# Kernel tuning notes

Measured on AMD Instinct MI355X. Metric: run time of the kernel, lower is better.

The kernel has to match this reference:

```python
import math
import jax, jax.numpy as jnp
import numpy as np

B, T, E, H, D = 4, 2048, 1024, 16, 64


def make_pe(max_len, d_model):
    pos = np.arange(max_len, dtype=np.float32)[:, None]
    div = np.exp(np.arange(0, d_model, 2, dtype=np.float32) * (-math.log(10000.0) / d_model))
    pe = np.zeros((max_len, d_model), dtype=np.float32)
    pe[:, 0::2] = np.sin(pos * div)
    pe[:, 1::2] = np.cos(pos * div)
    return jnp.asarray(pe)


def _rel_shift(x):
    # x: [T, K, B, H] -- Transformer-XL relative shift
    Tq, K, b, h = x.shape
    zp = jnp.zeros((Tq, 1, b, h), x.dtype)
    xp = jnp.concatenate([zp, x], axis=1).reshape(K + 1, Tq, b, h)
    return xp[1:].reshape(Tq, K, b, h)


def setup_inputs() -> dict:
    key = jax.random.key(0)
    ks = jax.random.split(key, 7)
    word_embedding = jax.random.normal(ks[0], (B, T, E), dtype=jnp.float32)
    lens = jax.random.randint(ks[1], (B,), 128, T + 1)  # >=128 so no empty softmax rows
    # torch Linear weights are [out, in]
    Wqkv = jax.random.normal(ks[2], (3 * H * D, E), dtype=jnp.float32) * (1.0 / math.sqrt(E))
    Wpos = jax.random.normal(ks[3], (H * D, E), dtype=jnp.float32) * (1.0 / math.sqrt(E))
    Wout = jax.random.normal(ks[4], (E, H * D), dtype=jnp.float32) * (1.0 / math.sqrt(H * D))
    bound = math.sqrt(6.0 / (H + D))  # xavier_uniform on [H, D]
    r_w_bias = jax.random.uniform(ks[5], (H, D), minval=-bound, maxval=bound, dtype=jnp.float32)
    r_r_bias = jax.random.uniform(ks[6], (H, D), minval=-bound, maxval=bound, dtype=jnp.float32)
    return {"word_embedding": word_embedding, "lens": lens, "Wqkv": Wqkv,
            "Wpos": Wpos, "Wout": Wout, "r_w_bias": r_w_bias, "r_r_bias": r_r_bias}


def reference(word_embedding, lens, Wqkv, Wpos, Wout, r_w_bias, r_r_bias):
    scale = 1.0 / math.sqrt(D)
    we = jnp.transpose(word_embedding, (1, 0, 2))  # [T, B, E]
    K = T  # mems=None
    pe = make_pe(K, E)  # [K, E], constant buffer

    heads = jnp.einsum('tbe,fe->tbf', we, Wqkv)  # [T, B, 3HD]
    q, k, v = jnp.split(heads, 3, axis=-1)
    q = q.reshape(T, B, H, D)
    k = k.reshape(K, B, H, D)
    v = v.reshape(K, B, H, D)
    Rk = (pe @ Wpos.T).reshape(K, H, D)  # [K, H, D]

    AC = jnp.einsum('ibnd,jbnd->ijbn', q + r_w_bias, k)   # [T, K, B, H]
    BD = _rel_shift(jnp.einsum('ibnd,jnd->ijbn', q + r_r_bias, Rk))
    score = (AC + BD) * scale

    # mask: key position j invalid if j >= lens[b]
    mask = jnp.arange(K)[:, None] >= lens[None, :]       # [K, B]
    score = jnp.where(mask[None, :, :, None], -1e30, score)
    prob = jax.nn.softmax(score, axis=1)

    vec = jnp.einsum('ijbn,jbnd->ibnd', prob, v).reshape(T, B, H * D)
    out = jnp.einsum('tbf,ef->tbe', vec, Wout)           # [T, B, E]
    return jnp.transpose(out, (1, 0, 2))                 # [B, T, E]
```

## Files before the change

### kernel.cpp

```cpp
#include <hip/hip_runtime.h>
#include <hip/hip_bf16.h>
#include <math.h>
#include <stdint.h>

constexpr int Bc  = 4;
constexpr int Tc  = 2048;
constexpr int Ec  = 1024;
constexpr int Hc  = 16;
constexpr int Dc  = 64;
constexpr int HDc = Hc * Dc;
constexpr int Kc  = Tc;
constexpr float SCL2E = 0.18033688011112042f;

typedef __bf16 bf16;
typedef __attribute__((ext_vector_type(8))) __bf16 bf16x8;
typedef __attribute__((ext_vector_type(4))) __bf16 bf16x4;
typedef __attribute__((ext_vector_type(4))) float f32x4;
typedef __attribute__((ext_vector_type(4))) _Float16 f16x4;

__device__ __forceinline__ void gload16(const bf16* gp, bf16* lp) {
  __builtin_amdgcn_global_load_lds(
      (const __attribute__((address_space(1))) void*)gp,
      (__attribute__((address_space(3))) void*)lp, 16, 0, 0);
}

constexpr int UN_WE   = 2097152;
constexpr int UN_QKV  = 786432;
constexpr int UN_WPOS = 262144;
constexpr int UN_WOUT = 262144;
constexpr int UN_PE   = 262144;
constexpr int UN_TOT  = UN_WE + UN_QKV + UN_WPOS + UN_WOUT + UN_PE;

__global__ __launch_bounds__(256) void prep_kernel(
    const float* __restrict__ we,   bf16* __restrict__ weH,
    const float* __restrict__ Wqkv, bf16* __restrict__ qkvH,
    const float* __restrict__ Wpos, bf16* __restrict__ WposH,
    const float* __restrict__ Wout, bf16* __restrict__ WoutH,
    bf16* __restrict__ WoutL,       bf16* __restrict__ peH) {
  int u = blockIdx.x * 256 + threadIdx.x;
  if (u >= UN_TOT) return;
  if (u < UN_WE + UN_QKV + UN_WPOS) {
    const float* src; bf16* dst; int i;
    if (u < UN_WE)                { src = we;   dst = weH;   i = u * 4; }
    else if (u < UN_WE + UN_QKV)  { src = Wqkv; dst = qkvH;  i = (u - UN_WE) * 4; }
    else                          { src = Wpos; dst = WposH; i = (u - UN_WE - UN_QKV) * 4; }
    float4 v = *(const float4*)(src + i);
    bf16x4 H = {(bf16)v.x, (bf16)v.y, (bf16)v.z, (bf16)v.w};
    *(bf16x4*)(dst + i) = H;
  } else if (u < UN_WE + UN_QKV + UN_WPOS + UN_WOUT) {
    int i = (u - UN_WE - UN_QKV - UN_WPOS) * 4;
    float4 v = *(const float4*)(Wout + i);
    bf16 h0 = (bf16)v.x, h1 = (bf16)v.y, h2 = (bf16)v.z, h3 = (bf16)v.w;
    bf16x4 H = {h0, h1, h2, h3};
    bf16x4 L = {(bf16)(v.x - (float)h0), (bf16)(v.y - (float)h1),
                (bf16)(v.z - (float)h2), (bf16)(v.w - (float)h3)};
    *(bf16x4*)(WoutH + i) = H;
    *(bf16x4*)(WoutL + i) = L;
  } else {
    int p4 = u - (UN_WE + UN_QKV + UN_WPOS + UN_WOUT);
    int pair0 = p4 * 4;
    int r = pair0 >> 9;
    int i = pair0 & 511;
    bf16x8 out;
#pragma unroll
    for (int k = 0; k < 4; k++) {
      float div = __expf((float)(i + k) * -0.017988946039015984f);
      float ang = (float)r * div;
      out[2 * k]     = (bf16)sinf(ang);
      out[2 * k + 1] = (bf16)cosf(ang);
    }
    *(bf16x8*)(peH + (size_t)r * Ec + 2 * i) = out;
  }
}

template <int EPI, int SPLIT>
__global__ __launch_bounds__(256) void gemm_mfma(
    const bf16* __restrict__ Ah_g, const bf16* __restrict__ Al_g,
    const bf16* __restrict__ Bh_g, const bf16* __restrict__ Bl_g,
    void* __restrict__ o0, void* __restrict__ o1,
    void* __restrict__ o2, void* __restrict__ o3,
    const float* __restrict__ rwb, const float* __restrict__ rrb,
    const int* __restrict__ lens_, int Kd) {
  const int bn = blockIdx.x * 128, bm = blockIdx.y * 128;
  if (EPI == 0) {
    if ((bn >> 10) != 0) {
      int bb = bm >> 11, t0 = bm & 2047;
      int lc = (lens_[bb] + 63) & ~63;
      if (t0 >= lc) return;
    }
  }
  const int tid = threadIdx.x, wv = tid >> 6, lane = tid & 63;
  const int wm = wv >> 1, wn = wv & 1;
  const int g = lane >> 4, laneL = lane & 15;

  __shared__ bf16 lds[(SPLIT ? 4 : 2) * 128 * 64];
  bf16* Ah = lds;
  bf16* Al = lds + 8192;
  bf16* Bh = lds + (SPLIT ? 16384 : 8192);
  bf16* Bl = lds + 24576;

  f32x4 acc[4][4];
#pragma unroll
  for (int fi = 0; fi < 4; fi++)
#pragma unroll
    for (int fj = 0; fj < 4; fj++) acc[fi][fj] = (f32x4){0.f, 0.f, 0.f, 0.f};

  const int rb  = lane >> 3;
  const int cb8 = ((lane & 7) ^ rb) * 8;
  const bf16* Abase_h = Ah_g + (size_t)bm * Kd;
  const bf16* Abase_l = SPLIT ? Al_g + (size_t)bm * Kd : nullptr;
  const bf16* Bbase_h = Bh_g + (size_t)bn * Kd;
  const bf16* Bbase_l = SPLIT ? Bl_g + (size_t)bn * Kd : nullptr;

  for (int k0 = 0; k0 < Kd; k0 += 64) {
    __syncthreads();
#pragma unroll
    for (int t = 0; t < 4; t++) {
      int r = t * 32 + wv * 8 + rb;
      size_t go = (size_t)r * Kd + k0 + cb8;
      int lo_ = (t * 32 + wv * 8) * 64;
      gload16(Abase_h + go, Ah + lo_);
      gload16(Bbase_h + go, Bh + lo_);
      if (SPLIT) {
        gload16(Abase_l + go, Al + lo_);
        gload16(Bbase_l + go, Bl + lo_);
      }
    }
    __syncthreads();
#pragma unroll
    for (int kk = 0; kk < 2; kk++) {
      bf16x8 afh[4], afl[4], bfh[4], bfl[4];
#pragma unroll
      for (int fi = 0; fi < 4; fi++) {
        int row = wm * 64 + fi * 16 + laneL;
        int off = row * 64 + (((kk * 4 + g) ^ (row & 7)) * 8);
        afh[fi] = *(const bf16x8*)(Ah + off);
        if (SPLIT) afl[fi] = *(const bf16x8*)(Al + off);
      }
#pragma unroll
      for (int fj = 0; fj < 4; fj++) {
        int row = wn * 64 + fj * 16 + laneL;
        int off = row * 64 + (((kk * 4 + g) ^ (row & 7)) * 8);
        bfh[fj] = *(const bf16x8*)(Bh + off);
        if (SPLIT) bfl[fj] = *(const bf16x8*)(Bl + off);
      }
#pragma unroll
      for (int fi = 0; fi < 4; fi++)
#pragma unroll
        for (int fj = 0; fj < 4; fj++) {
          acc[fi][fj] = __builtin_amdgcn_mfma_f32_16x16x32_bf16(afh[fi], bfh[fj], acc[fi][fj], 0, 0, 0);
          if (SPLIT) {
            acc[fi][fj] = __builtin_amdgcn_mfma_f32_16x16x32_bf16(afh[fi], bfl[fj], acc[fi][fj], 0, 0, 0);
            acc[fi][fj] = __builtin_amdgcn_mfma_f32_16x16x32_bf16(afl[fi], bfh[fj], acc[fi][fj], 0, 0, 0);
          }
        }
    }
  }

#pragma unroll
  for (int fi = 0; fi < 4; fi++) {
#pragma unroll
    for (int fj = 0; fj < 4; fj++) {
      int n = bn + wn * 64 + fj * 16 + laneL;
      int sec = n >> 10, f = n & 1023, hh = f >> 6, d = f & 63;
      float rw = 0.f, rr = 0.f;
      if (EPI == 0 && sec == 0) { rw = rwb[f]; rr = rrb[f]; }
#pragma unroll
      for (int rg = 0; rg < 4; rg++) {
        int m = bm + wm * 64 + fi * 16 + g * 4 + rg;
        float cv = acc[fi][fj][rg];
        if (EPI == 0) {
          int bb = m >> 11, t = m & 2047;
          if (sec == 0) {
            size_t o = (((size_t)(bb * Hc + hh)) * Tc + t) * 64 + d;
            ((bf16*)o0)[o] = (bf16)((cv + rw) * SCL2E);
            ((bf16*)o1)[o] = (bf16)((cv + rr) * SCL2E);
          } else if (sec == 1) {
            ((bf16*)o2)[(((size_t)(bb * Hc + hh)) * Tc + t) * 64 + d] = (bf16)cv;
          } else {
            ((bf16*)o3)[(((size_t)(bb * Hc + hh)) * 64 + d) * Tc + t] = (bf16)cv;
          }
        } else if (EPI == 1) {
          ((bf16*)o0)[((size_t)(n >> 6) * Kc + m) * 64 + (n & 63)] = (bf16)cv;
        } else {
          ((float*)o0)[(size_t)m * 1024 + n] = cv;
        }
      }
    }
  }
}

__global__ __launch_bounds__(256, 2) void attn_mfma(
    const bf16* __restrict__ qw, const bf16* __restrict__ qr,
    const bf16* __restrict__ kbuf, const bf16* __restrict__ vT,
    const bf16* __restrict__ Rk, const int* __restrict__ lens,
    bf16* __restrict__ vecH, bf16* __restrict__ vecL) {
  const int bid = blockIdx.x;
  const int h  = (bid & 7) * 2 + ((bid >> 3) & 1);
  const int i0 = ((bid >> 4) & 31) * 64;
  const int b  = bid >> 9;
  const int tid = threadIdx.x, wv = tid >> 6, lane = tid & 63;
  const int g = lane >> 4, laneL = lane & 15;
  const int len = lens[b];

  __shared__ __attribute__((aligned(16))) _Float16 Gs[4][16 * 84];
  __shared__ bf16 Kst[2][64 * 64];
  __shared__ bf16 Vst[2][64 * 64];

  const size_t bh = (size_t)(b * Hc + h) * Tc * 64;
  const bf16* qwB = qw   + bh;
  const bf16* qrB = qr   + bh;
  const bf16* kB  = kbuf + bh;
  const bf16* vTB = vT   + bh;
  const bf16* RkB = Rk   + (size_t)h * Kc * 64;

  const int myrow  = i0 + wv * 16 + laneL;
  const int myrow2 = (myrow + 1 < Tc) ? myrow + 1 : Tc - 1;
  bf16x8 bqw[2], bq1[2], bq2[2];
#pragma unroll
  for (int kk = 0; kk < 2; kk++) {
    bqw[kk] = *(const bf16x8*)(qwB + (size_t)myrow  * 64 + kk * 32 + g * 8);
    bq1[kk] = *(const bf16x8*)(qrB + (size_t)myrow  * 64 + kk * 32 + g * 8);
    bq2[kk] = *(const bf16x8*)(qrB + (size_t)myrow2 * 64 + kk * 32 + g * 8);
  }

  float m_ = -1e30f, l_ = 0.f;
  f32x4 O[4];
#pragma unroll
  for (int nf = 0; nf < 4; nf++) O[nf] = (f32x4){0.f, 0.f, 0.f, 0.f};

  _Float16* Gp = &Gs[wv][0];
  bf16*     Pp = (bf16*)&Gs[wv][0];
  const int pswz = (laneL & 7) << 3;

  auto stage = [&](int buf, int j0n) __attribute__((always_inline)) {
#pragma unroll
    for (int t = 0; t < 2; t++) {
      const int r0  = wv * 16 + t * 8;
      const int row = r0 + (lane >> 3);
      const int c8  = (lane & 7) ^ ((lane >> 3) & 7);
      gload16(kB  + (size_t)(j0n + row) * 64 + c8 * 8, &Kst[buf][r0 * 64]);
      gload16(vTB + (size_t)row * Tc + j0n + c8 * 8,   &Vst[buf][r0 * 64]);
    }
  };

  auto issue_rk = [&](bf16x8 (&rf)[10], int j0n) __attribute__((always_inline)) {
    const int cn = i0 - j0n;
    const int pb = (cn >= 0 ? Tc - 16 - cn : -cn - 17) - wv * 16;
#pragma unroll
    for (int mf = 0; mf < 5; mf++) {
      int p = pb + mf * 16 + laneL;
      p = p < 0 ? 0 : (p > Kc - 1 ? Kc - 1 : p);
#pragma unroll
      for (int kk = 0; kk < 2; kk++)
        rf[mf * 2 + kk] = *(const bf16x8*)(RkB + (size_t)p * 64 + kk * 32 + g * 8);
    }
  };

  auto compute_tile = [&](int cur, int j0c, const bf16x8 (&rf)[10])
      __attribute__((always_inline)) {
    const int c = i0 - j0c;
    const int swz8 = laneL & 7;

    f32x4 ST[4];
    __builtin_amdgcn_s_setprio(1);
#pragma unroll
    for (int nf = 0; nf < 4; nf++) {
      f32x4 acc = (f32x4){0.f, 0.f, 0.f, 0.f};
#pragma unroll
      for (int kk = 0; kk < 2; kk++) {
        bf16x8 bk = *(const bf16x8*)(&Kst[cur][(nf * 16 + laneL) * 64 + (((kk * 4 + g) ^ swz8) * 8)]);
        acc = __builtin_amdgcn_mfma_f32_16x16x32_bf16(bk, bqw[kk], acc, 0, 0, 0);
      }
      ST[nf] = acc;
    }
    __builtin_amdgcn_s_setprio(0);

    const int iic  = wv * 16 + laneL + c;
    const int colb = laneL * 84 + 15 - laneL;
    float P_[4][4];

    if (c > 0) {
      __builtin_amdgcn_s_setprio(1);
#pragma unroll
      for (int mf = 0; mf < 5; mf++) {
        f32x4 acc = (f32x4){0.f, 0.f, 0.f, 0.f};
#pragma unroll
        for (int kk = 0; kk < 2; kk++)
          acc = __builtin_amdgcn_mfma_f32_16x16x32_bf16(rf[mf * 2 + kk], bq1[kk], acc, 0, 0, 0);
        f16x4 gv = {(_Float16)acc[0], (_Float16)acc[1], (_Float16)acc[2], (_Float16)acc[3]};
        *(f16x4*)(Gp + laneL * 84 + mf * 16 + g * 4) = gv;
      }
      __builtin_amdgcn_s_setprio(0);
#pragma unroll
      for (int nf = 0; nf < 4; nf++)
#pragma unroll
        for (int r = 0; r < 4; r++)
          P_[nf][r] = (float)Gp[colb + nf * 16 + g * 4 + r];
    } else if (c < 0) {
      __builtin_amdgcn_s_setprio(1);
#pragma unroll
      for (int mf = 0; mf < 5; mf++) {
        f32x4 acc = (f32x4){0.f, 0.f, 0.f, 0.f};
#pragma unroll
        for (int kk = 0; kk < 2; kk++)
          acc = __builtin_amdgcn_mfma_f32_16x16x32_bf16(rf[mf * 2 + kk], bq2[kk], acc, 0, 0, 0);
        f16x4 gv = {(_Float16)acc[0], (_Float16)acc[1], (_Float16)acc[2], (_Float16)acc[3]};
        *(f16x4*)(Gp + laneL * 84 + mf * 16 + g * 4) = gv;
      }
      __builtin_amdgcn_s_setprio(0);
#pragma unroll
      for (int nf = 0; nf < 4; nf++)
#pragma unroll
        for (int r = 0; r < 4; r++) {
          const int jj = nf * 16 + g * 4 + r;
          float g2v = (float)Gp[colb + jj];
          P_[nf][r] = (jj == iic + 1) ? 0.f : g2v;
        }
    } else {
      __builtin_amdgcn_s_setprio(1);
#pragma unroll
      for (int mf = 0; mf < 5; mf++) {
        f32x4 acc = (f32x4){0.f, 0.f, 0.f, 0.f};
#pragma unroll
        for (int kk = 0; kk < 2; kk++)
          acc = __builtin_amdgcn_mfma_f32_16x16x32_bf16(rf[mf * 2 + kk], bq1[kk], acc, 0, 0, 0);
        f16x4 gv = {(_Float16)acc[0], (_Float16)acc[1], (_Float16)acc[2], (_Float16)acc[3]};
        *(f16x4*)(Gp + laneL * 84 + mf * 16 + g * 4) = gv;
      }
      __builtin_amdgcn_s_setprio(0);
#pragma unroll
      for (int nf = 0; nf < 4; nf++)
#pragma unroll
        for (int r = 0; r < 4; r++)
          P_[nf][r] = (float)Gp[colb + nf * 16 + g * 4 + r];
      const int pb = -17 - wv * 16;
      __builtin_amdgcn_s_setprio(1);
#pragma unroll
      for (int mf = 0; mf < 5; mf++) {
        int p = pb + mf * 16 + laneL;
        p = p < 0 ? 0 : (p > Kc - 1 ? Kc - 1 : p);
        f32x4 acc = (f32x4){0.f, 0.f, 0.f, 0.f};
#pragma unroll
        for (int kk = 0; kk < 2; kk++) {
          bf16x8 ark = *(const bf16x8*)(RkB + (size_t)p * 64 + kk * 32 + g * 8);
          acc = __builtin_amdgcn_mfma_f32_16x16x32_bf16(ark, bq2[kk], acc, 0, 0, 0);
        }
        f16x4 gv = {(_Float16)acc[0], (_Float16)acc[1], (_Float16)acc[2], (_Float16)acc[3]};
        *(f16x4*)(Gp + laneL * 84 + mf * 16 + g * 4) = gv;
      }
      __builtin_amdgcn_s_setprio(0);
#pragma unroll
      for (int nf = 0; nf < 4; nf++)
#pragma unroll
        for (int r = 0; r < 4; r++) {
          const int jj = nf * 16 + g * 4 + r;
          float g2v = (float)Gp[colb + jj];
          P_[nf][r] = (jj <= iic) ? P_[nf][r] : ((jj == iic + 1) ? 0.f : g2v);
        }
    }

    float pmax = -1e30f;
#pragma unroll
    for (int nf = 0; nf < 4; nf++)
#pragma unroll
      for (int r = 0; r < 4; r++) {
        float s = ST[nf][r] + P_[nf][r];
        P_[nf][r] = s;
        pmax = fmaxf(pmax, s);
      }
    if (j0c + 64 > len) {
#pragma unroll
      for (int nf = 0; nf < 4; nf++)
#pragma unroll
        for (int r = 0; r < 4; r++) {
          const int jj = nf * 16 + g * 4 + r;
          if (j0c + jj >= len) P_[nf][r] = -1e30f;
        }
      pmax = -1e30f;
#pragma unroll
      for (int nf = 0; nf < 4; nf++)
#pragma unroll
        for (int r = 0; r < 4; r++) pmax = fmaxf(pmax, P_[nf][r]);
    }

    if (__any(pmax > m_ + 8.0f)) {
      float rmax = fmaxf(pmax, __shfl_xor(pmax, 16));
      rmax = fmaxf(rmax, __shfl_xor(rmax, 32));
      const float mnew = fmaxf(m_, rmax);
      const float fac = exp2f(m_ - mnew);
      l_ *= fac;
#pragma unroll
      for (int nf = 0; nf < 4; nf++) O[nf] *= fac;
      m_ = mnew;
    }
    float sum = 0.f;
#pragma unroll
    for (int nf = 0; nf < 4; nf++)
#pragma unroll
      for (int r = 0; r < 4; r++) {
        float p = exp2f(P_[nf][r] - m_);
        P_[nf][r] = p;
        sum += p;
      }
    l_ += sum;

    asm volatile("" ::: "memory");
#pragma unroll
    for (int mf = 0; mf < 4; mf++) {
      bf16x4 pv = {(bf16)P_[mf][0], (bf16)P_[mf][1], (bf16)P_[mf][2], (bf16)P_[mf][3]};
      *(bf16x4*)(Pp + laneL * 64 + ((mf * 16 + g * 4) ^ pswz)) = pv;
    }

    __builtin_amdgcn_s_setprio(1);
#pragma unroll
    for (int kk = 0; kk < 2; kk++) {
      bf16x8 pbf = *(const bf16x8*)(Pp + laneL * 64 + ((kk * 32 + g * 8) ^ pswz));
#pragma unroll
      for (int nf = 0; nf < 4; nf++) {
        bf16x8 av = *(const bf16x8*)(&Vst[cur][(nf * 16 + laneL) * 64 + (((kk * 4 + g) ^ swz8) * 8)]);
        O[nf] = __builtin_amdgcn_mfma_f32_16x16x32_bf16(av, pbf, O[nf], 0, 0, 0);
      }
    }
    __builtin_amdgcn_s_setprio(0);
  };

  auto cbar = [&]() __attribute__((always_inline)) {
    __builtin_amdgcn_sched_barrier(0);
    asm volatile("s_waitcnt vmcnt(10)" ::: "memory");
    __builtin_amdgcn_s_barrier();
    __builtin_amdgcn_sched_barrier(0);
  };

  const int ntiles = (len + 63) >> 6;
  bf16x8 rfA[10], rfB[10];
  issue_rk(rfA, 0);
  stage(0, 0);
  __syncthreads();
  int cur = 0;
  for (int t = 0; t < ntiles; t += 2) {
    const int j0 = t << 6;
    if (t + 1 < ntiles) {
      stage(cur ^ 1, j0 + 64);
      __builtin_amdgcn_sched_barrier(0);
      issue_rk(rfB, j0 + 64);
      compute_tile(cur, j0, rfA);
      cbar();
    } else {
      compute_tile(cur, j0, rfA);
      __syncthreads();
    }
    cur ^= 1;
    if (t + 1 < ntiles) {
      if (t + 2 < ntiles) {
        stage(cur ^ 1, j0 + 128);
        __builtin_amdgcn_sched_barrier(0);
        issue_rk(rfA, j0 + 128);
        compute_tile(cur, j0 + 64, rfB);
        cbar();
      } else {
        compute_tile(cur, j0 + 64, rfB);
        __syncthreads();
      }
      cur ^= 1;
    }
  }

  float lrow = l_ + __shfl_xor(l_, 16);
  lrow += __shfl_xor(lrow, 32);
  const float inv = 1.0f / lrow;
  const size_t rowb = (size_t)(b * Tc + i0 + wv * 16 + laneL) * HDc + h * 64;
#pragma unroll
  for (int nf = 0; nf < 4; nf++) {
    float o0 = O[nf][0] * inv, o1 = O[nf][1] * inv,
          o2 = O[nf][2] * inv, o3 = O[nf][3] * inv;
    bf16x4 hv = {(bf16)o0, (bf16)o1, (bf16)o2, (bf16)o3};
    bf16x4 lv = {(bf16)(o0 - (float)hv[0]), (bf16)(o1 - (float)hv[1]),
                 (bf16)(o2 - (float)hv[2]), (bf16)(o3 - (float)hv[3])};
    *(bf16x4*)&vecH[rowb + nf * 16 + g * 4] = hv;
    *(bf16x4*)&vecL[rowb + nf * 16 + g * 4] = lv;
  }
}

extern "C" void kernel_launch(void* const* d_in, const int* in_sizes, int n_in,
                              void* d_out, int out_size, void* d_ws, size_t ws_size,
                              hipStream_t stream) {
  const float* we   = (const float*)d_in[0];
  const int*   lens = (const int*)  d_in[1];
  const float* Wqkv = (const float*)d_in[2];
  const float* Wpos = (const float*)d_in[3];
  const float* Wout = (const float*)d_in[4];
  const float* rwb  = (const float*)d_in[5];
  const float* rrb  = (const float*)d_in[6];
  float* out = (float*)d_out;

  bf16* ws = (bf16*)d_ws;
  const size_t BHTD = (size_t)Bc * Hc * Tc * Dc;
  bf16* qw    = ws;
  bf16* qr    = qw    + BHTD;
  bf16* kkp   = qr    + BHTD;
  bf16* vTp   = kkp   + BHTD;
  bf16* Rk    = vTp   + BHTD;
  bf16* peH   = Rk    + (size_t)Hc * Kc * Dc;
  bf16* weH   = peH   + (size_t)Kc * Ec;
  bf16* qkvH  = weH   + BHTD;
  bf16* WposH = qkvH  + (size_t)3 * HDc * Ec;
  bf16* WoutH = WposH + (size_t)HDc * Ec;
  bf16* WoutL = WoutH + (size_t)Ec * HDc;
  bf16* vecH  = WoutL + (size_t)Ec * HDc;
  bf16* vecL  = vecH  + BHTD;

  prep_kernel<<<(UN_TOT + 255) / 256, 256, 0, stream>>>(
      we, weH, Wqkv, qkvH, Wpos, WposH, Wout, WoutH, WoutL, peH);

  gemm_mfma<1, 0><<<dim3(HDc / 128, Kc / 128), 256, 0, stream>>>(
      peH, nullptr, WposH, nullptr, Rk, nullptr, nullptr, nullptr, nullptr, nullptr,
      nullptr, Ec);
  gemm_mfma<0, 0><<<dim3(3 * HDc / 128, (Bc * Tc) / 128), 256, 0, stream>>>(
      weH, nullptr, qkvH, nullptr, qw, qr, kkp, vTp, rwb, rrb, lens, Ec);
  attn_mfma<<<dim3(Tc / 64 * Hc * Bc), 256, 0, stream>>>(
      qw, qr, kkp, vTp, Rk, lens, vecH, vecL);
  gemm_mfma<2, 1><<<dim3(Ec / 128, (Bc * Tc) / 128), 256, 0, stream>>>(
      vecH, vecL, WoutH, WoutL, out, nullptr, nullptr, nullptr, nullptr, nullptr,
      nullptr, HDc);
}
```

Before: 464.4 us.

## Deepen K/V staging to four LDS buffers, prefetching two tiles ahead

The attention kernel now keeps four K/V tile buffers in LDS and stages two future tiles per iteration, so loads run two tiles ahead of compute. The Rk register prefetch is issued after each compute tile, and a single barrier per pair of tiles waits with a looser vmcnt. This is meant to hide more global-load latency and cut the number of barriers. In exchange, LDS use roughly doubles for K/V (about 64KB plus Gs), which may reduce occupancy below the two blocks per CU requested by launch bounds.

Result: faster. 453.5 us, median of 2 (-2.4%).

```diff
diff --git a/kernel.cpp b/kernel.cpp
--- a/kernel.cpp
+++ b/kernel.cpp
@@ -204,8 +204,8 @@
   const int len = lens[b];
 
   __shared__ __attribute__((aligned(16))) _Float16 Gs[4][16 * 84];
-  __shared__ bf16 Kst[2][64 * 64];
-  __shared__ bf16 Vst[2][64 * 64];
+  __shared__ bf16 Kst[4][64 * 64];
+  __shared__ bf16 Vst[4][64 * 64];
 
   const size_t bh = (size_t)(b * Hc + h) * Tc * 64;
   const bf16* qwB = qw   + bh;
@@ -425,7 +425,13 @@
     __builtin_amdgcn_s_setprio(0);
   };
 
-  auto cbar = [&]() __attribute__((always_inline)) {
+  auto cbar20 = [&]() __attribute__((always_inline)) {
+    __builtin_amdgcn_sched_barrier(0);
+    asm volatile("s_waitcnt vmcnt(20)" ::: "memory");
+    __builtin_amdgcn_s_barrier();
+    __builtin_amdgcn_sched_barrier(0);
+  };
+  auto cbar10 = [&]() __attribute__((always_inline)) {
     __builtin_amdgcn_sched_barrier(0);
     asm volatile("s_waitcnt vmcnt(10)" ::: "memory");
     __builtin_amdgcn_s_barrier();
@@ -434,36 +440,31 @@
 
   const int ntiles = (len + 63) >> 6;
   bf16x8 rfA[10], rfB[10];
+  stage(0, 0);
+  stage(1, 64);
   issue_rk(rfA, 0);
-  stage(0, 0);
+  issue_rk(rfB, 64);
   __syncthreads();
-  int cur = 0;
-  for (int t = 0; t < ntiles; t += 2) {
+  int t = 0;
+  for (; t + 1 < ntiles; t += 2) {
+    const int pp = (t >> 1) & 1;
+    const int bA = pp * 2, bB = pp * 2 + 1;
+    const int o2 = (pp ^ 1) * 2, o3 = o2 + 1;
     const int j0 = t << 6;
-    if (t + 1 < ntiles) {
-      stage(cur ^ 1, j0 + 64);
-      __builtin_amdgcn_sched_barrier(0);
-      issue_rk(rfB, j0 + 64);
-      compute_tile(cur, j0, rfA);
-      cbar();
-    } else {
-      compute_tile(cur, j0, rfA);
-      __syncthreads();
-    }
-    cur ^= 1;
-    if (t + 1 < ntiles) {
-      if (t + 2 < ntiles) {
-        stage(cur ^ 1, j0 + 128);
-        __builtin_amdgcn_sched_barrier(0);
-        issue_rk(rfA, j0 + 128);
-        compute_tile(cur, j0 + 64, rfB);
-        cbar();
-      } else {
-        compute_tile(cur, j0 + 64, rfB);
-        __syncthreads();
-      }
-      cur ^= 1;
-    }
+    const bool s2 = (t + 2 < ntiles), s3 = (t + 3 < ntiles);
+    if (s2) stage(o2, j0 + 128);
+    if (s3) stage(o3, j0 + 192);
+    __builtin_amdgcn_sched_barrier(0);
+    compute_tile(bA, j0, rfA);
+    if (s2) issue_rk(rfA, j0 + 128);
+    compute_tile(bB, j0 + 64, rfB);
+    if (s3) issue_rk(rfB, j0 + 192);
+    if (s3)      cbar20();
+    else if (s2) cbar10();
+  }
+  if (t < ntiles) {
+    const int pp = (t >> 1) & 1;
+    compute_tile(pp * 2, t << 6, rfA);
   }
 
   float lrow = l_ + __shfl_xor(l_, 16);
```
